# Optimization experiments

Measured on AMD Instinct MI355X. Metric: run time of the kernel, lower is better.

Reference implementation:

```python
import jax, jax.numpy as jnp
import numpy as np

B, S, HIDDEN = 4, 2048, 1024
NUM_EXPERTS = 8
TOP_K = 4
EPS = 1e-6


def setup_inputs() -> dict:
    key = jax.random.key(0)
    k0, k1, k2 = jax.random.split(key, 3)
    x = jax.random.normal(k0, (B, S, HIDDEN), dtype=jnp.float32)
    Wg = jax.random.normal(k1, (HIDDEN, NUM_EXPERTS), dtype=jnp.float32) * 0.02
    bg = jnp.zeros((NUM_EXPERTS,), dtype=jnp.float32)
    W = jax.random.normal(k2, (NUM_EXPERTS, HIDDEN, HIDDEN), dtype=jnp.float32) * 0.02
    b = jnp.zeros((NUM_EXPERTS, HIDDEN), dtype=jnp.float32)
    return {"x": x, "Wg": Wg, "bg": bg, "W": W, "b": b}


def reference(x, Wg, bg, W, b):
    Bb, Ss, D = x.shape
    xf = x.reshape(-1, D)                       # [T, D]
    T = xf.shape[0]

    # --- router ---
    router_logits = xf @ Wg + bg                # [T, E]
    router_probs = jax.nn.softmax(router_logits, axis=-1)
    top_k_probs, top_k_indices = jax.lax.top_k(router_probs, TOP_K)  # [T, K]
    top_k_weights = top_k_probs / (top_k_probs.sum(axis=-1, keepdims=True) + EPS)
    expert_mask = jax.nn.one_hot(top_k_indices, NUM_EXPERTS, dtype=jnp.float32).sum(axis=1)  # [T, E]

    # --- experts: original computes every expert on every token then masks;
    # same math expressed as one batched GEMM + gather ---
    all_out = jnp.einsum('td,edf->etf', xf, W) + b[:, None, :]  # [E, T, D]
    sel = all_out[top_k_indices.T, jnp.arange(T)[None, :]]      # [K, T, D]
    moe_output = jnp.einsum('tk,ktd->td', top_k_weights, sel).reshape(Bb, Ss, D)

    # --- load-balancing aux loss ---
    aux_loss = jnp.dot(expert_mask.mean(axis=0), router_probs.mean(axis=0)) * NUM_EXPERTS
    return moe_output, aux_loss
```

## Files before the change

kernel.cpp:

```cpp
#include <hip/hip_runtime.h>
#include <hip/hip_bf16.h>

#define T_TOK 8192
#define DH    1024
#define NE    8
#define TK    4

typedef unsigned short u16;
typedef __bf16 bf16x8 __attribute__((ext_vector_type(8)));
typedef float  f32x4  __attribute__((ext_vector_type(4)));

__device__ __forceinline__ u16 f2b(float f) {
    union { float f; unsigned u; } v; v.f = f;
    unsigned u = v.u;
    u += 0x7FFFu + ((u >> 16) & 1u);
    return (u16)(u >> 16);
}
__device__ __forceinline__ float b2f(u16 h) {
    union { unsigned u; float f; } v; v.u = ((unsigned)h) << 16;
    return v.f;
}
__device__ __forceinline__ void glds16(const u16* g, u16* l) {
    __builtin_amdgcn_global_load_lds((const __attribute__((address_space(1))) void*)g,
                                     (__attribute__((address_space(3))) void*)l, 16, 0, 0);
}

#define FENCE() asm volatile("" ::: "memory")
#define SBAR()  do { FENCE(); __builtin_amdgcn_s_barrier(); FENCE(); } while (0)
#define WAITLGKM0() do { asm volatile("s_waitcnt lgkmcnt(0)" ::: "memory"); \
                         __builtin_amdgcn_sched_barrier(0); } while (0)

__global__ __launch_bounds__(256) void cast_w_kernel(const float* __restrict__ W,
                                                     u16* __restrict__ wbt) {
    __shared__ float tile[64][65];
    const int e  = blockIdx.z;
    const int d0 = blockIdx.y * 64;
    const int f0 = blockIdx.x * 64;
    const int r  = threadIdx.x >> 4;
    const int c4 = (threadIdx.x & 15) * 4;
    const float* src = W + ((size_t)e << 20) + (size_t)d0 * DH + f0;
    #pragma unroll
    for (int i = 0; i < 4; i++) {
        const int row = i * 16 + r;
        const float4 v = *(const float4*)(src + (size_t)row * DH + c4);
        tile[row][c4]     = v.x;
        tile[row][c4 + 1] = v.y;
        tile[row][c4 + 2] = v.z;
        tile[row][c4 + 3] = v.w;
    }
    __syncthreads();
    u16* dst = wbt + ((size_t)e << 20) + (size_t)f0 * DH + d0;
    #pragma unroll
    for (int i = 0; i < 4; i++) {
        const int orow = i * 16 + r;
        ushort4 o;
        o.x = f2b(tile[c4][orow]);
        o.y = f2b(tile[c4 + 1][orow]);
        o.z = f2b(tile[c4 + 2][orow]);
        o.w = f2b(tile[c4 + 3][orow]);
        *(ushort4*)(dst + (size_t)orow * DH + c4) = o;
    }
}

__global__ __launch_bounds__(512) void router_kernel(
    const float* __restrict__ x, const float* __restrict__ Wg, const float* __restrict__ bg,
    u16* __restrict__ xb,
    int* __restrict__ bucket_tok, float* __restrict__ bucket_w,
    int* __restrict__ tk_e, float* __restrict__ tk_w,
    int* __restrict__ cnt, float* __restrict__ probsum)
{
    __shared__ int   lcnt[NE];
    __shared__ float lprob[NE];
    __shared__ int   gbase[NE];
    const int tid = threadIdx.x;
    const int wv = tid >> 6, lane = tid & 63;
    const int t = blockIdx.x * 8 + wv;
    if (tid < NE) { lcnt[tid] = 0; lprob[tid] = 0.f; }
    __syncthreads();

    float a[NE] = {};
    {
        const float* xr = x + (size_t)t * DH;
        u16* xbr = xb + (size_t)t * DH;
        const float4* wg = (const float4*)Wg;
        #pragma unroll
        for (int it = 0; it < 4; it++) {
            const int d = it * 256 + lane * 4;
            const float4 v = *(const float4*)(xr + d);
            ushort4 o;
            o.x = f2b(v.x); o.y = f2b(v.y); o.z = f2b(v.z); o.w = f2b(v.w);
            *(ushort4*)(xbr + d) = o;
            const float4 w0l = wg[2 * (d + 0)], w0h = wg[2 * (d + 0) + 1];
            const float4 w1l = wg[2 * (d + 1)], w1h = wg[2 * (d + 1) + 1];
            const float4 w2l = wg[2 * (d + 2)], w2h = wg[2 * (d + 2) + 1];
            const float4 w3l = wg[2 * (d + 3)], w3h = wg[2 * (d + 3) + 1];
            a[0] += v.x * w0l.x + v.y * w1l.x + v.z * w2l.x + v.w * w3l.x;
            a[1] += v.x * w0l.y + v.y * w1l.y + v.z * w2l.y + v.w * w3l.y;
            a[2] += v.x * w0l.z + v.y * w1l.z + v.z * w2l.z + v.w * w3l.z;
            a[3] += v.x * w0l.w + v.y * w1l.w + v.z * w2l.w + v.w * w3l.w;
            a[4] += v.x * w0h.x + v.y * w1h.x + v.z * w2h.x + v.w * w3h.x;
            a[5] += v.x * w0h.y + v.y * w1h.y + v.z * w2h.y + v.w * w3h.y;
            a[6] += v.x * w0h.z + v.y * w1h.z + v.z * w2h.z + v.w * w3h.z;
            a[7] += v.x * w0h.w + v.y * w1h.w + v.z * w2h.w + v.w * w3h.w;
        }
    }
    #pragma unroll
    for (int e = 0; e < NE; e++) {
        float v = a[e];
        #pragma unroll
        for (int off = 32; off > 0; off >>= 1) v += __shfl_down(v, off);
        a[e] = v;
    }

    int idx4[TK]; float w4[TK]; int off4[TK];
    if (lane == 0) {
        float logits[NE], probs[NE];
        float mx = -1e30f;
        #pragma unroll
        for (int e = 0; e < NE; e++) { logits[e] = a[e] + bg[e]; mx = fmaxf(mx, logits[e]); }
        float Z = 0.f;
        #pragma unroll
        for (int e = 0; e < NE; e++) { probs[e] = expf(logits[e] - mx); Z += probs[e]; }
        const float rZ = 1.f / Z;
        #pragma unroll
        for (int e = 0; e < NE; e++) probs[e] *= rZ;

        float rem2[NE];
        #pragma unroll
        for (int e = 0; e < NE; e++) rem2[e] = probs[e];
        float s4 = 0.f;
        #pragma unroll
        for (int k = 0; k < TK; k++) {
            int best = 0; float bv = rem2[0];
            #pragma unroll
            for (int e = 1; e < NE; e++) if (rem2[e] > bv) { bv = rem2[e]; best = e; }
            idx4[k] = best; w4[k] = bv; s4 += bv; rem2[best] = -1e30f;
        }
        const float rs = 1.f / (s4 + 1e-6f);
        #pragma unroll
        for (int k = 0; k < TK; k++) {
            w4[k] *= rs;
            tk_e[t * TK + k] = idx4[k];
            tk_w[t * TK + k] = w4[k];
            off4[k] = atomicAdd(&lcnt[idx4[k]], 1);
        }
        #pragma unroll
        for (int e = 0; e < NE; e++) atomicAdd(&lprob[e], probs[e]);
    }
    __syncthreads();
    if (tid < NE) {
        gbase[tid] = atomicAdd(&cnt[tid], lcnt[tid]);
        atomicAdd(&probsum[tid], lprob[tid]);
    }
    __syncthreads();
    if (lane == 0) {
        #pragma unroll
        for (int k = 0; k < TK; k++) {
            const int e = idx4[k];
            const int slot = gbase[e] + off4[k];
            bucket_tok[e * T_TOK + slot] = (t << 2) | k;
            bucket_w[e * T_TOK + slot]   = w4[k];
        }
    }
}

__global__ __launch_bounds__(512, 2) void moe_gemm_kernel(
    const u16* __restrict__ xb, const u16* __restrict__ wbt,
    const int* __restrict__ bucket_tok, const float* __restrict__ bucket_w,
    const int* __restrict__ cnt, u16* __restrict__ y)
{
    __shared__ u16 As[2][256 * 64];
    __shared__ u16 Bs[2][256 * 64];
    __shared__ int   s_tok[256];
    __shared__ float s_w[256];

    const int tid  = threadIdx.x;
    const int lane = tid & 63;
    const int wid  = tid >> 6;
    const int wr   = wid >> 2;
    const int wc   = wid & 3;
    const int fr   = lane & 15;
    const int fq   = (lane >> 4) * 8;
    const int swz  = (fr & 7) << 3;
    const int gsw  = ((lane & 7) ^ (lane >> 3)) * 8;
    const int crow = lane >> 3;

    const int ALb = 2 * wid + (wid >= 4 ? 8 : 0);
    const int AHb = ALb + 8;
    const int BLb = (wid >> 1) * 8 + (wid & 1) * 2;
    const int BHb = BLb + 4;

    const int e = blockIdx.x & 7;
    const int c = blockIdx.x >> 3;
    const int M = cnt[e];

    for (int j = 0; j < 4; ++j) {
        const int idx = j * 32 + c;
        const int mb = idx >> 2;
        const int nb = idx & 3;
        const int m0 = mb << 8;
        if (m0 >= M) continue;
        const int n0 = nb << 8;

        __syncthreads();
        if (tid < 256) {
            const int slot = m0 + tid;
            if (slot < M) {
                s_tok[tid] = bucket_tok[e * T_TOK + slot];
                s_w[tid]   = bucket_w[e * T_TOK + slot];
            } else { s_tok[tid] = -1; s_w[tid] = 0.f; }
        }
        __syncthreads();

        const int rAL0 = ALb * 8 + crow, rAL1 = rAL0 + 8;
        const int rAH0 = AHb * 8 + crow, rAH1 = rAH0 + 8;
        const int tAL0 = s_tok[rAL0], tAL1 = s_tok[rAL1];
        const int tAH0 = s_tok[rAH0], tAH1 = s_tok[rAH1];
        const u16* gAL0 = xb + (size_t)(tAL0 >= 0 ? (tAL0 >> 2) : 0) * DH + gsw;
        const u16* gAL1 = xb + (size_t)(tAL1 >= 0 ? (tAL1 >> 2) : 0) * DH + gsw;
        const u16* gAH0 = xb + (size_t)(tAH0 >= 0 ? (tAH0 >> 2) : 0) * DH + gsw;
        const u16* gAH1 = xb + (size_t)(tAH1 >= 0 ? (tAH1 >> 2) : 0) * DH + gsw;
        const u16* wbe  = wbt + ((size_t)e << 20);
        const u16* gBL0 = wbe + (size_t)(n0 + BLb * 8 + crow) * DH + gsw;
        const u16* gBL1 = gBL0 + (size_t)8 * DH;
        const u16* gBH0 = wbe + (size_t)(n0 + BHb * 8 + crow) * DH + gsw;
        const u16* gBH1 = gBH0 + (size_t)8 * DH;

        f32x4 acc[8][4] = {};

        #pragma unroll
        for (int kt = 0; kt < 2; kt++) {
            const int ko = kt * 64; const int p = kt;
            glds16(gAL0 + ko, &As[p][ALb * 512]); glds16(gAL1 + ko, &As[p][(ALb + 1) * 512]);
            glds16(gAH0 + ko, &As[p][AHb * 512]); glds16(gAH1 + ko, &As[p][(AHb + 1) * 512]);
            glds16(gBL0 + ko, &Bs[p][BLb * 512]); glds16(gBL1 + ko, &Bs[p][(BLb + 1) * 512]);
            glds16(gBH0 + ko, &Bs[p][BHb * 512]); glds16(gBH1 + ko, &Bs[p][(BHb + 1) * 512]);
        }
        asm volatile("s_waitcnt vmcnt(8)" ::: "memory");
        SBAR();

        const int arow = (wr * 128 + fr) * 64;
        const int brow = (wc * 64  + fr) * 64;
        const int c0 = fq ^ swz;
        const int c1 = (32 + fq) ^ swz;

        bf16x8 afL[4][2], afH[4][2], bfL[2][2], bfH[2][2];

        for (int kt = 0; kt < 16; ++kt) {
            const int p = kt & 1;
            const u16* Ap = &As[p][0];
            const u16* Bp = &Bs[p][0];

            #pragma unroll
            for (int mi = 0; mi < 4; mi++) {
                afL[mi][0] = *(const bf16x8*)&Ap[arow + mi * 1024 + c0];
                afL[mi][1] = *(const bf16x8*)&Ap[arow + mi * 1024 + c1];
            }
            #pragma unroll
            for (int nj = 0; nj < 2; nj++) {
                bfL[nj][0] = *(const bf16x8*)&Bp[brow + nj * 1024 + c0];
                bfL[nj][1] = *(const bf16x8*)&Bp[brow + nj * 1024 + c1];
            }
            if (kt >= 1 && kt <= 14) {
                const int ko = (kt + 1) * 64; const int q = (kt + 1) & 1;
                glds16(gAH0 + ko, &As[q][AHb * 512]);
                glds16(gAH1 + ko, &As[q][(AHb + 1) * 512]);
            }
            asm volatile("s_waitcnt lgkmcnt(8)" ::: "memory");
            SBAR(); WAITLGKM0();
            __builtin_amdgcn_s_setprio(1);
            #pragma unroll
            for (int mi = 0; mi < 4; mi++)
                #pragma unroll
                for (int nj = 0; nj < 2; nj++) {
                    acc[mi][nj] = __builtin_amdgcn_mfma_f32_16x16x32_bf16(afL[mi][0], bfL[nj][0], acc[mi][nj], 0, 0, 0);
                    acc[mi][nj] = __builtin_amdgcn_mfma_f32_16x16x32_bf16(afL[mi][1], bfL[nj][1], acc[mi][nj], 0, 0, 0);
                }
            __builtin_amdgcn_s_setprio(0);
            SBAR();

            #pragma unroll
            for (int nj = 0; nj < 2; nj++) {
                bfH[nj][0] = *(const bf16x8*)&Bp[brow + (nj + 2) * 1024 + c0];
                bfH[nj][1] = *(const bf16x8*)&Bp[brow + (nj + 2) * 1024 + c1];
            }
            if (kt <= 13) {
                const int ko = (kt + 2) * 64;
                glds16(gAL0 + ko, &As[p][ALb * 512]);
                glds16(gAL1 + ko, &As[p][(ALb + 1) * 512]);
            }
            SBAR(); WAITLGKM0();
            __builtin_amdgcn_s_setprio(1);
            #pragma unroll
            for (int mi = 0; mi < 4; mi++)
                #pragma unroll
                for (int nj = 0; nj < 2; nj++) {
                    acc[mi][nj + 2] = __builtin_amdgcn_mfma_f32_16x16x32_bf16(afL[mi][0], bfH[nj][0], acc[mi][nj + 2], 0, 0, 0);
                    acc[mi][nj + 2] = __builtin_amdgcn_mfma_f32_16x16x32_bf16(afL[mi][1], bfH[nj][1], acc[mi][nj + 2], 0, 0, 0);
                }
            __builtin_amdgcn_s_setprio(0);
            SBAR();

            #pragma unroll
            for (int mi = 0; mi < 4; mi++) {
                afH[mi][0] = *(const bf16x8*)&Ap[arow + (mi + 4) * 1024 + c0];
                afH[mi][1] = *(const bf16x8*)&Ap[arow + (mi + 4) * 1024 + c1];
            }
            if (kt <= 13) {
                const int ko = (kt + 2) * 64;
                glds16(gBL0 + ko, &Bs[p][BLb * 512]);
                glds16(gBL1 + ko, &Bs[p][(BLb + 1) * 512]);
            }
            SBAR(); WAITLGKM0();
            __builtin_amdgcn_s_setprio(1);
            #pragma unroll
            for (int mi = 0; mi < 4; mi++)
                #pragma unroll
                for (int nj = 0; nj < 2; nj++) {
                    acc[mi + 4][nj + 2] = __builtin_amdgcn_mfma_f32_16x16x32_bf16(afH[mi][0], bfH[nj][0], acc[mi + 4][nj + 2], 0, 0, 0);
                    acc[mi + 4][nj + 2] = __builtin_amdgcn_mfma_f32_16x16x32_bf16(afH[mi][1], bfH[nj][1], acc[mi + 4][nj + 2], 0, 0, 0);
                }
            __builtin_amdgcn_s_setprio(0);
            SBAR();

            if (kt <= 13) {
                const int ko = (kt + 2) * 64;
                glds16(gBH0 + ko, &Bs[p][BHb * 512]);
                glds16(gBH1 + ko, &Bs[p][(BHb + 1) * 512]);
            }
            __builtin_amdgcn_s_setprio(1);
            #pragma unroll
            for (int mi = 0; mi < 4; mi++)
                #pragma unroll
                for (int nj = 0; nj < 2; nj++) {
                    acc[mi + 4][nj] = __builtin_amdgcn_mfma_f32_16x16x32_bf16(afH[mi][0], bfL[nj][0], acc[mi + 4][nj], 0, 0, 0);
                    acc[mi + 4][nj] = __builtin_amdgcn_mfma_f32_16x16x32_bf16(afH[mi][1], bfL[nj][1], acc[mi + 4][nj], 0, 0, 0);
                }
            __builtin_amdgcn_s_setprio(0);
            if (kt <= 13)      asm volatile("s_waitcnt vmcnt(6)" ::: "memory");
            else if (kt == 14) asm volatile("s_waitcnt vmcnt(0)" ::: "memory");
            SBAR();
        }

        const int cl = lane & 15;
        const int rb = (lane >> 4) * 4;
        #pragma unroll
        for (int mi = 0; mi < 8; mi++) {
            #pragma unroll
            for (int r = 0; r < 4; r++) {
                const int srow = wr * 128 + mi * 16 + rb + r;
                const int tok = s_tok[srow];
                if (tok < 0) continue;
                const float w = s_w[srow];
                u16* yr = y + (size_t)tok * DH + (n0 + wc * 64 + cl);
                #pragma unroll
                for (int nj = 0; nj < 4; nj++)
                    yr[nj * 16] = f2b(acc[mi][nj][r] * w);
            }
        }
    }
}

__global__ __launch_bounds__(256) void combine_kernel(
    const u16* __restrict__ y, const int* __restrict__ tk_e, const float* __restrict__ tk_w,
    const float* __restrict__ bexp,
    const int* __restrict__ cnt, const float* __restrict__ probsum,
    float* __restrict__ out, float* __restrict__ out_aux)
{
    const int t = blockIdx.x;
    const int c = threadIdx.x * 4;
    if (t == 0 && threadIdx.x == 0) {
        float s = 0.f;
        for (int e = 0; e < NE; e++) s += (float)cnt[e] * probsum[e];
        out_aux[0] = s * (float)NE / ((float)T_TOK * (float)T_TOK);
    }
    float o0 = 0.f, o1 = 0.f, o2 = 0.f, o3 = 0.f;
    #pragma unroll
    for (int k = 0; k < TK; k++) {
        const int e   = tk_e[t * TK + k];
        const float w = tk_w[t * TK + k];
        const ushort4 yv = *(const ushort4*)(y + ((size_t)(t * TK + k)) * DH + c);
        const float4  bv = *(const float4*)(bexp + (size_t)e * DH + c);
        o0 += b2f(yv.x) + w * bv.x;
        o1 += b2f(yv.y) + w * bv.y;
        o2 += b2f(yv.z) + w * bv.z;
        o3 += b2f(yv.w) + w * bv.w;
    }
    float4 ov = {o0, o1, o2, o3};
    *(float4*)(out + (size_t)t * DH + c) = ov;
}

extern "C" void kernel_launch(void* const* d_in, const int* in_sizes, int n_in,
                              void* d_out, int out_size, void* d_ws, size_t ws_size,
                              hipStream_t stream)
{
    const float* x  = (const float*)d_in[0];
    const float* Wg = (const float*)d_in[1];
    const float* bg = (const float*)d_in[2];
    const float* W  = (const float*)d_in[3];
    const float* b  = (const float*)d_in[4];
    float* out = (float*)d_out;

    char* ws = (char*)d_ws;
    u16*   xb         = (u16*)(ws);
    u16*   wbt        = (u16*)(ws + 16777216);
    u16*   y          = (u16*)(ws + 33554432);
    int*   bucket_tok = (int*)(ws + 100663296);
    float* bucket_w   = (float*)(ws + 100925440);
    int*   tk_e       = (int*)(ws + 101187584);
    float* tk_w       = (float*)(ws + 101318656);
    int*   cnt        = (int*)(ws + 101449728);
    float* probsum    = (float*)(ws + 101449760);

    hipMemsetAsync(cnt, 0, 64, stream);

    cast_w_kernel<<<dim3(16, 16, NE), 256, 0, stream>>>(W, wbt);
    router_kernel<<<1024, 512, 0, stream>>>(x, Wg, bg, xb, bucket_tok, bucket_w, tk_e, tk_w, cnt, probsum);
    moe_gemm_kernel<<<dim3(256), 512, 0, stream>>>(xb, wbt, bucket_tok, bucket_w, cnt, y);
    combine_kernel<<<8192, 256, 0, stream>>>(y, tk_e, tk_w, b, cnt, probsum, out, out + (size_t)T_TOK * DH);
}
```

Before: 256.4 us.

## Fuse cast, router, expert GEMM and combine into one cooperative persistent kernel

Replaces four separate kernel launches (weight cast/transpose, router, grouped expert GEMM, combine) with a single cooperative kernel of 256 blocks that runs each phase in turn, separated by grid-wide syncs. This is meant to remove launch gaps and tail idling between the short phases. In exchange, the cast, router and combine phases now run on only 256 blocks of 512 threads with serial loops, which cuts their parallelism and latency hiding. Grid.sync also adds barrier cost and requires every block to be co-resident.

```diff
diff --git a/kernel.cpp b/kernel.cpp
--- a/kernel.cpp
+++ b/kernel.cpp
@@ -1,5 +1,8 @@
 #include <hip/hip_runtime.h>
 #include <hip/hip_bf16.h>
+#include <hip/hip_cooperative_groups.h>
+
+namespace cg = cooperative_groups;
 
 #define T_TOK 8192
 #define DH    1024
@@ -29,365 +32,383 @@
 #define SBAR()  do { FENCE(); __builtin_amdgcn_s_barrier(); FENCE(); } while (0)
 #define WAITLGKM0() do { asm volatile("s_waitcnt lgkmcnt(0)" ::: "memory"); \
                          __builtin_amdgcn_sched_barrier(0); } while (0)
-
-__global__ __launch_bounds__(256) void cast_w_kernel(const float* __restrict__ W,
-                                                     u16* __restrict__ wbt) {
-    __shared__ float tile[64][65];
-    const int e  = blockIdx.z;
-    const int d0 = blockIdx.y * 64;
-    const int f0 = blockIdx.x * 64;
-    const int r  = threadIdx.x >> 4;
-    const int c4 = (threadIdx.x & 15) * 4;
-    const float* src = W + ((size_t)e << 20) + (size_t)d0 * DH + f0;
-    #pragma unroll
-    for (int i = 0; i < 4; i++) {
-        const int row = i * 16 + r;
-        const float4 v = *(const float4*)(src + (size_t)row * DH + c4);
-        tile[row][c4]     = v.x;
-        tile[row][c4 + 1] = v.y;
-        tile[row][c4 + 2] = v.z;
-        tile[row][c4 + 3] = v.w;
-    }
-    __syncthreads();
-    u16* dst = wbt + ((size_t)e << 20) + (size_t)f0 * DH + d0;
-    #pragma unroll
-    for (int i = 0; i < 4; i++) {
-        const int orow = i * 16 + r;
-        ushort4 o;
-        o.x = f2b(tile[c4][orow]);
-        o.y = f2b(tile[c4 + 1][orow]);
-        o.z = f2b(tile[c4 + 2][orow]);
-        o.w = f2b(tile[c4 + 3][orow]);
-        *(ushort4*)(dst + (size_t)orow * DH + c4) = o;
-    }
-}
-
-__global__ __launch_bounds__(512) void router_kernel(
-    const float* __restrict__ x, const float* __restrict__ Wg, const float* __restrict__ bg,
-    u16* __restrict__ xb,
+#define WAITVM(n) asm volatile("s_waitcnt vmcnt(" #n ")" ::: "memory")
+
+__global__ __launch_bounds__(512, 2) void moe_fused_kernel(
+    const float* __restrict__ W, const float* __restrict__ x,
+    const float* __restrict__ Wg, const float* __restrict__ bg,
+    const float* __restrict__ bexp,
+    u16* __restrict__ xb, u16* __restrict__ wbt, u16* __restrict__ y,
     int* __restrict__ bucket_tok, float* __restrict__ bucket_w,
     int* __restrict__ tk_e, float* __restrict__ tk_w,
-    int* __restrict__ cnt, float* __restrict__ probsum)
-{
-    __shared__ int   lcnt[NE];
-    __shared__ float lprob[NE];
-    __shared__ int   gbase[NE];
-    const int tid = threadIdx.x;
-    const int wv = tid >> 6, lane = tid & 63;
-    const int t = blockIdx.x * 8 + wv;
-    if (tid < NE) { lcnt[tid] = 0; lprob[tid] = 0.f; }
-    __syncthreads();
-
-    float a[NE] = {};
-    {
-        const float* xr = x + (size_t)t * DH;
-        u16* xbr = xb + (size_t)t * DH;
-        const float4* wg = (const float4*)Wg;
-        #pragma unroll
-        for (int it = 0; it < 4; it++) {
-            const int d = it * 256 + lane * 4;
-            const float4 v = *(const float4*)(xr + d);
-            ushort4 o;
-            o.x = f2b(v.x); o.y = f2b(v.y); o.z = f2b(v.z); o.w = f2b(v.w);
-            *(ushort4*)(xbr + d) = o;
-            const float4 w0l = wg[2 * (d + 0)], w0h = wg[2 * (d + 0) + 1];
-            const float4 w1l = wg[2 * (d + 1)], w1h = wg[2 * (d + 1) + 1];
-            const float4 w2l = wg[2 * (d + 2)], w2h = wg[2 * (d + 2) + 1];
-            const float4 w3l = wg[2 * (d + 3)], w3h = wg[2 * (d + 3) + 1];
-            a[0] += v.x * w0l.x + v.y * w1l.x + v.z * w2l.x + v.w * w3l.x;
-            a[1] += v.x * w0l.y + v.y * w1l.y + v.z * w2l.y + v.w * w3l.y;
-            a[2] += v.x * w0l.z + v.y * w1l.z + v.z * w2l.z + v.w * w3l.z;
-            a[3] += v.x * w0l.w + v.y * w1l.w + v.z * w2l.w + v.w * w3l.w;
-            a[4] += v.x * w0h.x + v.y * w1h.x + v.z * w2h.x + v.w * w3h.x;
-            a[5] += v.x * w0h.y + v.y * w1h.y + v.z * w2h.y + v.w * w3h.y;
-            a[6] += v.x * w0h.z + v.y * w1h.z + v.z * w2h.z + v.w * w3h.z;
-            a[7] += v.x * w0h.w + v.y * w1h.w + v.z * w2h.w + v.w * w3h.w;
-        }
-    }
-    #pragma unroll
-    for (int e = 0; e < NE; e++) {
-        float v = a[e];
-        #pragma unroll
-        for (int off = 32; off > 0; off >>= 1) v += __shfl_down(v, off);
-        a[e] = v;
-    }
-
-    int idx4[TK]; float w4[TK]; int off4[TK];
-    if (lane == 0) {
-        float logits[NE], probs[NE];
-        float mx = -1e30f;
-        #pragma unroll
-        for (int e = 0; e < NE; e++) { logits[e] = a[e] + bg[e]; mx = fmaxf(mx, logits[e]); }
-        float Z = 0.f;
-        #pragma unroll
-        for (int e = 0; e < NE; e++) { probs[e] = expf(logits[e] - mx); Z += probs[e]; }
-        const float rZ = 1.f / Z;
-        #pragma unroll
-        for (int e = 0; e < NE; e++) probs[e] *= rZ;
-
-        float rem2[NE];
-        #pragma unroll
-        for (int e = 0; e < NE; e++) rem2[e] = probs[e];
-        float s4 = 0.f;
-        #pragma unroll
-        for (int k = 0; k < TK; k++) {
-            int best = 0; float bv = rem2[0];
-            #pragma unroll
-            for (int e = 1; e < NE; e++) if (rem2[e] > bv) { bv = rem2[e]; best = e; }
-            idx4[k] = best; w4[k] = bv; s4 += bv; rem2[best] = -1e30f;
-        }
-        const float rs = 1.f / (s4 + 1e-6f);
-        #pragma unroll
-        for (int k = 0; k < TK; k++) {
-            w4[k] *= rs;
-            tk_e[t * TK + k] = idx4[k];
-            tk_w[t * TK + k] = w4[k];
-            off4[k] = atomicAdd(&lcnt[idx4[k]], 1);
-        }
-        #pragma unroll
-        for (int e = 0; e < NE; e++) atomicAdd(&lprob[e], probs[e]);
-    }
-    __syncthreads();
-    if (tid < NE) {
-        gbase[tid] = atomicAdd(&cnt[tid], lcnt[tid]);
-        atomicAdd(&probsum[tid], lprob[tid]);
-    }
-    __syncthreads();
-    if (lane == 0) {
-        #pragma unroll
-        for (int k = 0; k < TK; k++) {
-            const int e = idx4[k];
-            const int slot = gbase[e] + off4[k];
-            bucket_tok[e * T_TOK + slot] = (t << 2) | k;
-            bucket_w[e * T_TOK + slot]   = w4[k];
-        }
-    }
-}
-
-__global__ __launch_bounds__(512, 2) void moe_gemm_kernel(
-    const u16* __restrict__ xb, const u16* __restrict__ wbt,
-    const int* __restrict__ bucket_tok, const float* __restrict__ bucket_w,
-    const int* __restrict__ cnt, u16* __restrict__ y)
+    int* __restrict__ cnt, float* __restrict__ probsum,
+    float* __restrict__ out)
 {
     __shared__ u16 As[2][256 * 64];
     __shared__ u16 Bs[2][256 * 64];
     __shared__ int   s_tok[256];
     __shared__ float s_w[256];
+    __shared__ int   lcnt[NE];
+    __shared__ float lprob[NE];
+    __shared__ int   gbase[NE];
 
     const int tid  = threadIdx.x;
     const int lane = tid & 63;
     const int wid  = tid >> 6;
-    const int wr   = wid >> 2;
-    const int wc   = wid & 3;
-    const int fr   = lane & 15;
-    const int fq   = (lane >> 4) * 8;
-    const int swz  = (fr & 7) << 3;
-    const int gsw  = ((lane & 7) ^ (lane >> 3)) * 8;
-    const int crow = lane >> 3;
-
-    const int ALb = 2 * wid + (wid >= 4 ? 8 : 0);
-    const int AHb = ALb + 8;
-    const int BLb = (wid >> 1) * 8 + (wid & 1) * 2;
-    const int BHb = BLb + 4;
-
-    const int e = blockIdx.x & 7;
-    const int c = blockIdx.x >> 3;
-    const int M = cnt[e];
-
-    for (int j = 0; j < 4; ++j) {
-        const int idx = j * 32 + c;
-        const int mb = idx >> 2;
-        const int nb = idx & 3;
-        const int m0 = mb << 8;
-        if (m0 >= M) continue;
-        const int n0 = nb << 8;
-
+    const int bid  = blockIdx.x;
+
+    cg::grid_group grid = cg::this_grid();
+
+    if (tid < NE) { lcnt[tid] = 0; lprob[tid] = 0.f; }
+
+    {
+        const int half = tid >> 8;
+        const int tloc = tid & 255;
+        const int r  = tloc >> 4;
+        const int c4 = (tloc & 15) * 4;
+        float* tb = (float*)&As[0][0];
+        float (*tile)[65] = (float(*)[65])(tb + half * (64 * 65));
+        #pragma unroll 1
+        for (int rd = 0; rd < 4; ++rd) {
+            const int jc = bid * 8 + rd * 2 + half;
+            const int f0 = (jc & 15) * 64;
+            const int d0 = ((jc >> 4) & 15) * 64;
+            const int e  = jc >> 8;
+            const float* src = W + ((size_t)e << 20) + (size_t)d0 * DH + f0;
+            #pragma unroll
+            for (int i = 0; i < 4; i++) {
+                const int row = i * 16 + r;
+                const float4 v = *(const float4*)(src + (size_t)row * DH + c4);
+                tile[row][c4]     = v.x;
+                tile[row][c4 + 1] = v.y;
+                tile[row][c4 + 2] = v.z;
+                tile[row][c4 + 3] = v.w;
+            }
+            __syncthreads();
+            u16* dst = wbt + ((size_t)e << 20) + (size_t)f0 * DH + d0;
+            #pragma unroll
+            for (int i = 0; i < 4; i++) {
+                const int orow = i * 16 + r;
+                ushort4 o;
+                o.x = f2b(tile[c4][orow]);
+                o.y = f2b(tile[c4 + 1][orow]);
+                o.z = f2b(tile[c4 + 2][orow]);
+                o.w = f2b(tile[c4 + 3][orow]);
+                *(ushort4*)(dst + (size_t)orow * DH + c4) = o;
+            }
+            __syncthreads();
+        }
+    }
+
+    {
+        const int g = bid * 8 + wid;
+        int   ridx[4][TK]; float rww[4][TK]; int roff[4][TK];
+        const float4* wg = (const float4*)Wg;
+        #pragma unroll
+        for (int rr = 0; rr < 4; ++rr) {
+            const int t = g * 4 + rr;
+            float a[NE] = {};
+            const float* xr = x + (size_t)t * DH;
+            u16* xbr = xb + (size_t)t * DH;
+            #pragma unroll
+            for (int it = 0; it < 4; it++) {
+                const int d = it * 256 + lane * 4;
+                const float4 v = *(const float4*)(xr + d);
+                ushort4 o;
+                o.x = f2b(v.x); o.y = f2b(v.y); o.z = f2b(v.z); o.w = f2b(v.w);
+                *(ushort4*)(xbr + d) = o;
+                const float4 w0l = wg[2 * (d + 0)], w0h = wg[2 * (d + 0) + 1];
+                const float4 w1l = wg[2 * (d + 1)], w1h = wg[2 * (d + 1) + 1];
+                const float4 w2l = wg[2 * (d + 2)], w2h = wg[2 * (d + 2) + 1];
+                const float4 w3l = wg[2 * (d + 3)], w3h = wg[2 * (d + 3) + 1];
+                a[0] += v.x * w0l.x + v.y * w1l.x + v.z * w2l.x + v.w * w3l.x;
+                a[1] += v.x * w0l.y + v.y * w1l.y + v.z * w2l.y + v.w * w3l.y;
+                a[2] += v.x * w0l.z + v.y * w1l.z + v.z * w2l.z + v.w * w3l.z;
+                a[3] += v.x * w0l.w + v.y * w1l.w + v.z * w2l.w + v.w * w3l.w;
+                a[4] += v.x * w0h.x + v.y * w1h.x + v.z * w2h.x + v.w * w3h.x;
+                a[5] += v.x * w0h.y + v.y * w1h.y + v.z * w2h.y + v.w * w3h.y;
+                a[6] += v.x * w0h.z + v.y * w1h.z + v.z * w2h.z + v.w * w3h.z;
+                a[7] += v.x * w0h.w + v.y * w1h.w + v.z * w2h.w + v.w * w3h.w;
+            }
+            #pragma unroll
+            for (int ee = 0; ee < NE; ee++) {
+                float v = a[ee];
+                #pragma unroll
+                for (int off = 32; off > 0; off >>= 1) v += __shfl_down(v, off);
+                a[ee] = v;
+            }
+            if (lane == 0) {
+                float logits[NE], probs[NE];
+                float mx = -1e30f;
+                #pragma unroll
+                for (int ee = 0; ee < NE; ee++) { logits[ee] = a[ee] + bg[ee]; mx = fmaxf(mx, logits[ee]); }
+                float Z = 0.f;
+                #pragma unroll
+                for (int ee = 0; ee < NE; ee++) { probs[ee] = expf(logits[ee] - mx); Z += probs[ee]; }
+                const float rZ = 1.f / Z;
+                #pragma unroll
+                for (int ee = 0; ee < NE; ee++) probs[ee] *= rZ;
+
+                float rem2[NE];
+                #pragma unroll
+                for (int ee = 0; ee < NE; ee++) rem2[ee] = probs[ee];
+                float s4 = 0.f;
+                #pragma unroll
+                for (int k = 0; k < TK; k++) {
+                    int best = 0; float bv = rem2[0];
+                    #pragma unroll
+                    for (int ee = 1; ee < NE; ee++) if (rem2[ee] > bv) { bv = rem2[ee]; best = ee; }
+                    ridx[rr][k] = best; rww[rr][k] = bv; s4 += bv; rem2[best] = -1e30f;
+                }
+                const float rs = 1.f / (s4 + 1e-6f);
+                #pragma unroll
+                for (int k = 0; k < TK; k++) {
+                    rww[rr][k] *= rs;
+                    tk_e[t * TK + k] = ridx[rr][k];
+                    tk_w[t * TK + k] = rww[rr][k];
+                    roff[rr][k] = atomicAdd(&lcnt[ridx[rr][k]], 1);
+                }
+                #pragma unroll
+                for (int ee = 0; ee < NE; ee++) atomicAdd(&lprob[ee], probs[ee]);
+            }
+        }
         __syncthreads();
-        if (tid < 256) {
-            const int slot = m0 + tid;
-            if (slot < M) {
-                s_tok[tid] = bucket_tok[e * T_TOK + slot];
-                s_w[tid]   = bucket_w[e * T_TOK + slot];
-            } else { s_tok[tid] = -1; s_w[tid] = 0.f; }
+        if (tid < NE) {
+            gbase[tid] = atomicAdd(&cnt[tid], lcnt[tid]);
+            atomicAdd(&probsum[tid], lprob[tid]);
         }
         __syncthreads();
-
-        const int rAL0 = ALb * 8 + crow, rAL1 = rAL0 + 8;
-        const int rAH0 = AHb * 8 + crow, rAH1 = rAH0 + 8;
-        const int tAL0 = s_tok[rAL0], tAL1 = s_tok[rAL1];
-        const int tAH0 = s_tok[rAH0], tAH1 = s_tok[rAH1];
-        const u16* gAL0 = xb + (size_t)(tAL0 >= 0 ? (tAL0 >> 2) : 0) * DH + gsw;
-        const u16* gAL1 = xb + (size_t)(tAL1 >= 0 ? (tAL1 >> 2) : 0) * DH + gsw;
-        const u16* gAH0 = xb + (size_t)(tAH0 >= 0 ? (tAH0 >> 2) : 0) * DH + gsw;
-        const u16* gAH1 = xb + (size_t)(tAH1 >= 0 ? (tAH1 >> 2) : 0) * DH + gsw;
-        const u16* wbe  = wbt + ((size_t)e << 20);
-        const u16* gBL0 = wbe + (size_t)(n0 + BLb * 8 + crow) * DH + gsw;
-        const u16* gBL1 = gBL0 + (size_t)8 * DH;
-        const u16* gBH0 = wbe + (size_t)(n0 + BHb * 8 + crow) * DH + gsw;
-        const u16* gBH1 = gBH0 + (size_t)8 * DH;
-
-        f32x4 acc[8][4] = {};
-
-        #pragma unroll
-        for (int kt = 0; kt < 2; kt++) {
-            const int ko = kt * 64; const int p = kt;
-            glds16(gAL0 + ko, &As[p][ALb * 512]); glds16(gAL1 + ko, &As[p][(ALb + 1) * 512]);
-            glds16(gAH0 + ko, &As[p][AHb * 512]); glds16(gAH1 + ko, &As[p][(AHb + 1) * 512]);
-            glds16(gBL0 + ko, &Bs[p][BLb * 512]); glds16(gBL1 + ko, &Bs[p][(BLb + 1) * 512]);
-            glds16(gBH0 + ko, &Bs[p][BHb * 512]); glds16(gBH1 + ko, &Bs[p][(BHb + 1) * 512]);
-        }
-        asm volatile("s_waitcnt vmcnt(8)" ::: "memory");
-        SBAR();
-
-        const int arow = (wr * 128 + fr) * 64;
-        const int brow = (wc * 64  + fr) * 64;
-        const int c0 = fq ^ swz;
-        const int c1 = (32 + fq) ^ swz;
-
-        bf16x8 afL[4][2], afH[4][2], bfL[2][2], bfH[2][2];
-
-        for (int kt = 0; kt < 16; ++kt) {
-            const int p = kt & 1;
-            const u16* Ap = &As[p][0];
-            const u16* Bp = &Bs[p][0];
-
-            #pragma unroll
-            for (int mi = 0; mi < 4; mi++) {
-                afL[mi][0] = *(const bf16x8*)&Ap[arow + mi * 1024 + c0];
-                afL[mi][1] = *(const bf16x8*)&Ap[arow + mi * 1024 + c1];
-            }
-            #pragma unroll
-            for (int nj = 0; nj < 2; nj++) {
-                bfL[nj][0] = *(const bf16x8*)&Bp[brow + nj * 1024 + c0];
-                bfL[nj][1] = *(const bf16x8*)&Bp[brow + nj * 1024 + c1];
-            }
-            if (kt >= 1 && kt <= 14) {
-                const int ko = (kt + 1) * 64; const int q = (kt + 1) & 1;
-                glds16(gAH0 + ko, &As[q][AHb * 512]);
-                glds16(gAH1 + ko, &As[q][(AHb + 1) * 512]);
-            }
-            asm volatile("s_waitcnt lgkmcnt(8)" ::: "memory");
-            SBAR(); WAITLGKM0();
-            __builtin_amdgcn_s_setprio(1);
-            #pragma unroll
-            for (int mi = 0; mi < 4; mi++)
+        if (lane == 0) {
+            #pragma unroll
+            for (int rr = 0; rr < 4; ++rr)
+                #pragma unroll
+                for (int k = 0; k < TK; k++) {
+                    const int ee = ridx[rr][k];
+                    const int slot = gbase[ee] + roff[rr][k];
+                    bucket_tok[ee * T_TOK + slot] = ((g * 4 + rr) << 2) | k;
+                    bucket_w[ee * T_TOK + slot]   = rww[rr][k];
+                }
+        }
+    }
+
+    __threadfence();
+    grid.sync();
+
+    {
+        const int wr   = wid >> 2;
+        const int wc   = wid & 3;
+        const int fr   = lane & 15;
+        const int fq   = (lane >> 4) * 8;
+        const int swz  = (fr & 7) << 3;
+        const int gsw  = ((lane & 7) ^ (lane >> 3)) * 8;
+        const int crow = lane >> 3;
+
+        const int ALb = 2 * wid + (wid >= 4 ? 8 : 0);
+        const int AHb = ALb + 8;
+        const int BLb = (wid >> 1) * 8 + (wid & 1) * 2;
+        const int BHb = BLb + 4;
+
+        const int eg = bid & 7;
+        const int cc = bid >> 3;
+        const int M  = cnt[eg];
+
+        for (int j = 0; j < 4; ++j) {
+            const int idx = j * 32 + cc;
+            const int mb = idx >> 2;
+            const int nb = idx & 3;
+            const int m0 = mb << 8;
+            if (m0 >= M) continue;
+            const int n0 = nb << 8;
+
+            __syncthreads();
+            if (tid < 256) {
+                const int slot = m0 + tid;
+                if (slot < M) {
+                    s_tok[tid] = bucket_tok[eg * T_TOK + slot];
+                    s_w[tid]   = bucket_w[eg * T_TOK + slot];
+                } else { s_tok[tid] = -1; s_w[tid] = 0.f; }
+            }
+            __syncthreads();
+
+            const int rAL0 = ALb * 8 + crow, rAL1 = rAL0 + 8;
+            const int rAH0 = AHb * 8 + crow, rAH1 = rAH0 + 8;
+            const int tAL0 = s_tok[rAL0], tAL1 = s_tok[rAL1];
+            const int tAH0 = s_tok[rAH0], tAH1 = s_tok[rAH1];
+            const u16* gAL0 = xb + (size_t)(tAL0 >= 0 ? (tAL0 >> 2) : 0) * DH + gsw;
+            const u16* gAL1 = xb + (size_t)(tAL1 >= 0 ? (tAL1 >> 2) : 0) * DH + gsw;
+            const u16* gAH0 = xb + (size_t)(tAH0 >= 0 ? (tAH0 >> 2) : 0) * DH + gsw;
+            const u16* gAH1 = xb + (size_t)(tAH1 >= 0 ? (tAH1 >> 2) : 0) * DH + gsw;
+            const u16* wbe  = wbt + ((size_t)eg << 20);
+            const u16* gBL0 = wbe + (size_t)(n0 + BLb * 8 + crow) * DH + gsw;
+            const u16* gBL1 = gBL0 + (size_t)8 * DH;
+            const u16* gBH0 = wbe + (size_t)(n0 + BHb * 8 + crow) * DH + gsw;
+            const u16* gBH1 = gBH0 + (size_t)8 * DH;
+
+            f32x4 acc[8][4] = {};
+
+            #pragma unroll
+            for (int kt = 0; kt < 2; kt++) {
+                const int ko = kt * 64; const int p = kt;
+                glds16(gAL0 + ko, &As[p][ALb * 512]); glds16(gAL1 + ko, &As[p][(ALb + 1) * 512]);
+                glds16(gAH0 + ko, &As[p][AHb * 512]); glds16(gAH1 + ko, &As[p][(AHb + 1) * 512]);
+                glds16(gBL0 + ko, &Bs[p][BLb * 512]); glds16(gBL1 + ko, &Bs[p][(BLb + 1) * 512]);
+                glds16(gBH0 + ko, &Bs[p][BHb * 512]); glds16(gBH1 + ko, &Bs[p][(BHb + 1) * 512]);
+            }
+            WAITVM(8);
+            SBAR();
+
+            const int arow = (wr * 128 + fr) * 64;
+            const int brow = (wc * 64  + fr) * 64;
+            const int c0 = fq ^ swz;
+            const int c1 = (32 + fq) ^ swz;
+
+            bf16x8 afL[4][2], afH[4][2], bfL[2][2], bfH[2][2];
+
+            for (int kt = 0; kt < 16; ++kt) {
+                const int p = kt & 1;
+                const u16* Ap = &As[p][0];
+                const u16* Bp = &Bs[p][0];
+
+                #pragma unroll
+                for (int mi = 0; mi < 4; mi++) {
+                    afL[mi][0] = *(const bf16x8*)&Ap[arow + mi * 1024 + c0];
+                    afL[mi][1] = *(const bf16x8*)&Ap[arow + mi * 1024 + c1];
+                }
                 #pragma unroll
                 for (int nj = 0; nj < 2; nj++) {
-                    acc[mi][nj] = __builtin_amdgcn_mfma_f32_16x16x32_bf16(afL[mi][0], bfL[nj][0], acc[mi][nj], 0, 0, 0);
-                    acc[mi][nj] = __builtin_amdgcn_mfma_f32_16x16x32_bf16(afL[mi][1], bfL[nj][1], acc[mi][nj], 0, 0, 0);
-                }
-            __builtin_amdgcn_s_setprio(0);
-            SBAR();
-
-            #pragma unroll
-            for (int nj = 0; nj < 2; nj++) {
-                bfH[nj][0] = *(const bf16x8*)&Bp[brow + (nj + 2) * 1024 + c0];
-                bfH[nj][1] = *(const bf16x8*)&Bp[brow + (nj + 2) * 1024 + c1];
-            }
-            if (kt <= 13) {
-                const int ko = (kt + 2) * 64;
-                glds16(gAL0 + ko, &As[p][ALb * 512]);
-                glds16(gAL1 + ko, &As[p][(ALb + 1) * 512]);
-            }
-            SBAR(); WAITLGKM0();
-            __builtin_amdgcn_s_setprio(1);
-            #pragma unroll
-            for (int mi = 0; mi < 4; mi++)
+                    bfL[nj][0] = *(const bf16x8*)&Bp[brow + nj * 1024 + c0];
+                    bfL[nj][1] = *(const bf16x8*)&Bp[brow + nj * 1024 + c1];
+                }
+                if (kt >= 1 && kt <= 14) {
+                    const int ko = (kt + 1) * 64; const int q = (kt + 1) & 1;
+                    glds16(gAH0 + ko, &As[q][AHb * 512]);
+                    glds16(gAH1 + ko, &As[q][(AHb + 1) * 512]);
+                }
+                asm volatile("s_waitcnt lgkmcnt(8)" ::: "memory");
+                SBAR(); WAITLGKM0();
+                __builtin_amdgcn_s_setprio(1);
+                #pragma unroll
+                for (int mi = 0; mi < 4; mi++)
+                    #pragma unroll
+                    for (int nj = 0; nj < 2; nj++) {
+                        acc[mi][nj] = __builtin_amdgcn_mfma_f32_16x16x32_bf16(afL[mi][0], bfL[nj][0], acc[mi][nj], 0, 0, 0);
+                        acc[mi][nj] = __builtin_amdgcn_mfma_f32_16x16x32_bf16(afL[mi][1], bfL[nj][1], acc[mi][nj], 0, 0, 0);
+                    }
+                __builtin_amdgcn_s_setprio(0);
+                SBAR();
+
                 #pragma unroll
                 for (int nj = 0; nj < 2; nj++) {
-                    acc[mi][nj + 2] = __builtin_amdgcn_mfma_f32_16x16x32_bf16(afL[mi][0], bfH[nj][0], acc[mi][nj + 2], 0, 0, 0);
-                    acc[mi][nj + 2] = __builtin_amdgcn_mfma_f32_16x16x32_bf16(afL[mi][1], bfH[nj][1], acc[mi][nj + 2], 0, 0, 0);
-                }
-            __builtin_amdgcn_s_setprio(0);
-            SBAR();
-
-            #pragma unroll
-            for (int mi = 0; mi < 4; mi++) {
-                afH[mi][0] = *(const bf16x8*)&Ap[arow + (mi + 4) * 1024 + c0];
-                afH[mi][1] = *(const bf16x8*)&Ap[arow + (mi + 4) * 1024 + c1];
-            }
-            if (kt <= 13) {
-                const int ko = (kt + 2) * 64;
-                glds16(gBL0 + ko, &Bs[p][BLb * 512]);
-                glds16(gBL1 + ko, &Bs[p][(BLb + 1) * 512]);
-            }
-            SBAR(); WAITLGKM0();
-            __builtin_amdgcn_s_setprio(1);
-            #pragma unroll
-            for (int mi = 0; mi < 4; mi++)
-                #pragma unroll
-                for (int nj = 0; nj < 2; nj++) {
-                    acc[mi + 4][nj + 2] = __builtin_amdgcn_mfma_f32_16x16x32_bf16(afH[mi][0], bfH[nj][0], acc[mi + 4][nj + 2], 0, 0, 0);
-                    acc[mi + 4][nj + 2] = __builtin_amdgcn_mfma_f32_16x16x32_bf16(afH[mi][1], bfH[nj][1], acc[mi + 4][nj + 2], 0, 0, 0);
-                }
-            __builtin_amdgcn_s_setprio(0);
-            SBAR();
-
-            if (kt <= 13) {
-                const int ko = (kt + 2) * 64;
-                glds16(gBH0 + ko, &Bs[p][BHb * 512]);
-                glds16(gBH1 + ko, &Bs[p][(BHb + 1) * 512]);
-            }
-            __builtin_amdgcn_s_setprio(1);
-            #pragma unroll
-            for (int mi = 0; mi < 4; mi++)
-                #pragma unroll
-                for (int nj = 0; nj < 2; nj++) {
-                    acc[mi + 4][nj] = __builtin_amdgcn_mfma_f32_16x16x32_bf16(afH[mi][0], bfL[nj][0], acc[mi + 4][nj], 0, 0, 0);
-                    acc[mi + 4][nj] = __builtin_amdgcn_mfma_f32_16x16x32_bf16(afH[mi][1], bfL[nj][1], acc[mi + 4][nj], 0, 0, 0);
-                }
-            __builtin_amdgcn_s_setprio(0);
-            if (kt <= 13)      asm volatile("s_waitcnt vmcnt(6)" ::: "memory");
-            else if (kt == 14) asm volatile("s_waitcnt vmcnt(0)" ::: "memory");
-            SBAR();
-        }
-
-        const int cl = lane & 15;
-        const int rb = (lane >> 4) * 4;
-        #pragma unroll
-        for (int mi = 0; mi < 8; mi++) {
-            #pragma unroll
-            for (int r = 0; r < 4; r++) {
-                const int srow = wr * 128 + mi * 16 + rb + r;
-                const int tok = s_tok[srow];
-                if (tok < 0) continue;
-                const float w = s_w[srow];
-                u16* yr = y + (size_t)tok * DH + (n0 + wc * 64 + cl);
-                #pragma unroll
-                for (int nj = 0; nj < 4; nj++)
-                    yr[nj * 16] = f2b(acc[mi][nj][r] * w);
+                    bfH[nj][0] = *(const bf16x8*)&Bp[brow + (nj + 2) * 1024 + c0];
+                    bfH[nj][1] = *(const bf16x8*)&Bp[brow + (nj + 2) * 1024 + c1];
+                }
+                if (kt <= 13) {
+                    const int ko = (kt + 2) * 64;
+                    glds16(gAL0 + ko, &As[p][ALb * 512]);
+                    glds16(gAL1 + ko, &As[p][(ALb + 1) * 512]);
+                }
+                SBAR(); WAITLGKM0();
+                __builtin_amdgcn_s_setprio(1);
+                #pragma unroll
+                for (int mi = 0; mi < 4; mi++)
+                    #pragma unroll
+                    for (int nj = 0; nj < 2; nj++) {
+                        acc[mi][nj + 2] = __builtin_amdgcn_mfma_f32_16x16x32_bf16(afL[mi][0], bfH[nj][0], acc[mi][nj + 2], 0, 0, 0);
+                        acc[mi][nj + 2] = __builtin_amdgcn_mfma_f32_16x16x32_bf16(afL[mi][1], bfH[nj][1], acc[mi][nj + 2], 0, 0, 0);
+                    }
+                __builtin_amdgcn_s_setprio(0);
+                SBAR();
+
+                #pragma unroll
+                for (int mi = 0; mi < 4; mi++) {
+                    afH[mi][0] = *(const bf16x8*)&Ap[arow + (mi + 4) * 1024 + c0];
+                    afH[mi][1] = *(const bf16x8*)&Ap[arow + (mi + 4) * 1024 + c1];
+                }
+                if (kt <= 13) {
+                    const int ko = (kt + 2) * 64;
+                    glds16(gBL0 + ko, &Bs[p][BLb * 512]);
+                    glds16(gBL1 + ko, &Bs[p][(BLb + 1) * 512]);
+                }
+                SBAR(); WAITLGKM0();
+                __builtin_amdgcn_s_setprio(1);
+                #pragma unroll
+                for (int mi = 0; mi < 4; mi++)
+                    #pragma unroll
+                    for (int nj = 0; nj < 2; nj++) {
+                        acc[mi + 4][nj + 2] = __builtin_amdgcn_mfma_f32_16x16x32_bf16(afH[mi][0], bfH[nj][0], acc[mi + 4][nj + 2], 0, 0, 0);
+                        acc[mi + 4][nj + 2] = __builtin_amdgcn_mfma_f32_16x16x32_bf16(afH[mi][1], bfH[nj][1], acc[mi + 4][nj + 2], 0, 0, 0);
+                    }
+                __builtin_amdgcn_s_setprio(0);
+                SBAR();
+
+                if (kt <= 13) {
+                    const int ko = (kt + 2) * 64;
+                    glds16(gBH0 + ko, &Bs[p][BHb * 512]);
+                    glds16(gBH1 + ko, &Bs[p][(BHb + 1) * 512]);
+                }
+                __builtin_amdgcn_s_setprio(1);
+                #pragma unroll
+                for (int mi = 0; mi < 4; mi++)
+                    #pragma unroll
+                    for (int nj = 0; nj < 2; nj++) {
+                        acc[mi + 4][nj] = __builtin_amdgcn_mfma_f32_16x16x32_bf16(afH[mi][0], bfL[nj][0], acc[mi + 4][nj], 0, 0, 0);
+                        acc[mi + 4][nj] = __builtin_amdgcn_mfma_f32_16x16x32_bf16(afH[mi][1], bfL[nj][1], acc[mi + 4][nj], 0, 0, 0);
+                    }
+                __builtin_amdgcn_s_setprio(0);
+                if (kt <= 13)      WAITVM(6);
+                else if (kt == 14) WAITVM(0);
+                SBAR();
+            }
+
+            const int cl = lane & 15;
+            const int rb = (lane >> 4) * 4;
+            #pragma unroll
+            for (int mi = 0; mi < 8; mi++) {
+                #pragma unroll
+                for (int r = 0; r < 4; r++) {
+                    const int srow = wr * 128 + mi * 16 + rb + r;
+                    const int tok = s_tok[srow];
+                    if (tok < 0) continue;
+                    const float w = s_w[srow];
+                    u16* yr = y + (size_t)tok * DH + (n0 + wc * 64 + cl);
+                    #pragma unroll
+                    for (int nj = 0; nj < 4; nj++)
+                        yr[nj * 16] = f2b(acc[mi][nj][r] * w);
+                }
             }
         }
     }
-}
-
-__global__ __launch_bounds__(256) void combine_kernel(
-    const u16* __restrict__ y, const int* __restrict__ tk_e, const float* __restrict__ tk_w,
-    const float* __restrict__ bexp,
-    const int* __restrict__ cnt, const float* __restrict__ probsum,
-    float* __restrict__ out, float* __restrict__ out_aux)
-{
-    const int t = blockIdx.x;
-    const int c = threadIdx.x * 4;
-    if (t == 0 && threadIdx.x == 0) {
-        float s = 0.f;
-        for (int e = 0; e < NE; e++) s += (float)cnt[e] * probsum[e];
-        out_aux[0] = s * (float)NE / ((float)T_TOK * (float)T_TOK);
+
+    __threadfence();
+    grid.sync();
+
+    {
+        if (bid == 0 && tid == 0) {
+            float s = 0.f;
+            for (int ee = 0; ee < NE; ee++) s += (float)cnt[ee] * probsum[ee];
+            out[(size_t)T_TOK * DH] = s * (float)NE / ((float)T_TOK * (float)T_TOK);
+        }
+        const int s2 = tid >> 8;
+        const int c  = (tid & 255) * 4;
+        #pragma unroll 1
+        for (int i = 0; i < 16; ++i) {
+            const int t = bid * 32 + i * 2 + s2;
+            float o0 = 0.f, o1 = 0.f, o2 = 0.f, o3 = 0.f;
+            #pragma unroll
+            for (int k = 0; k < TK; k++) {
+                const int ee  = tk_e[t * TK + k];
+                const float w = tk_w[t * TK + k];
+                const ushort4 yv = *(const ushort4*)(y + ((size_t)(t * TK + k)) * DH + c);
+                const float4  bv = *(const float4*)(bexp + (size_t)ee * DH + c);
+                o0 += b2f(yv.x) + w * bv.x;
+                o1 += b2f(yv.y) + w * bv.y;
+                o2 += b2f(yv.z) + w * bv.z;
+                o3 += b2f(yv.w) + w * bv.w;
+            }
+            float4 ov = {o0, o1, o2, o3};
+            *(float4*)(out + (size_t)t * DH + c) = ov;
+        }
     }
-    float o0 = 0.f, o1 = 0.f, o2 = 0.f, o3 = 0.f;
-    #pragma unroll
-    for (int k = 0; k < TK; k++) {
-        const int e   = tk_e[t * TK + k];
-        const float w = tk_w[t * TK + k];
-        const ushort4 yv = *(const ushort4*)(y + ((size_t)(t * TK + k)) * DH + c);
-        const float4  bv = *(const float4*)(bexp + (size_t)e * DH + c);
-        o0 += b2f(yv.x) + w * bv.x;
-        o1 += b2f(yv.y) + w * bv.y;
-        o2 += b2f(yv.z) + w * bv.z;
-        o3 += b2f(yv.w) + w * bv.w;
-    }
-    float4 ov = {o0, o1, o2, o3};
-    *(float4*)(out + (size_t)t * DH + c) = ov;
 }
 
 extern "C" void kernel_launch(void* const* d_in, const int* in_sizes, int n_in,
@@ -414,8 +435,13 @@
 
     hipMemsetAsync(cnt, 0, 64, stream);
 
-    cast_w_kernel<<<dim3(16, 16, NE), 256, 0, stream>>>(W, wbt);
-    router_kernel<<<1024, 512, 0, stream>>>(x, Wg, bg, xb, bucket_tok, bucket_w, tk_e, tk_w, cnt, probsum);
-    moe_gemm_kernel<<<dim3(256), 512, 0, stream>>>(xb, wbt, bucket_tok, bucket_w, cnt, y);
-    combine_kernel<<<8192, 256, 0, stream>>>(y, tk_e, tk_w, b, cnt, probsum, out, out + (size_t)T_TOK * DH);
+    void* params[] = {
+        (void*)&W, (void*)&x, (void*)&Wg, (void*)&bg, (void*)&b,
+        (void*)&xb, (void*)&wbt, (void*)&y,
+        (void*)&bucket_tok, (void*)&bucket_w,
+        (void*)&tk_e, (void*)&tk_w,
+        (void*)&cnt, (void*)&probsum, (void*)&out
+    };
+    (void)hipLaunchCooperativeKernel((const void*)moe_fused_kernel,
+                                     dim3(256), dim3(512), params, 0, stream);
 }
```

Measured after the change: 432.5 us. 68.7% more time.
